# Kernel optimization log

Measured on AMD Instinct MI355X. Metric: run time of the kernel, lower is better.

The kernel has to match this reference:

```python
import jax, jax.numpy as jnp
import numpy as np
from jax import lax

Z, Y, X = 9, 5, 5          # anchor grid (AnchorInit)
A = Z * Y * X              # 225 anchors
NS = 8                     # nsample in AnchorGrouping
H = 64                     # feature / hidden width


def anchor_template():
    # (Z,Y,X,3) grid of anchor coordinates, last dim ordered (x,y,z) so that
    # anchors[:,:,:2] += g_loc shifts the planar (x,y) location.
    xs = (jnp.arange(X, dtype=jnp.float32) - (X - 1) / 2.0) * 0.2
    ys = (jnp.arange(Y, dtype=jnp.float32) - (Y - 1) / 2.0) * 0.2
    zs = jnp.arange(Z, dtype=jnp.float32) * 0.22 + 0.1
    gz, gy, gx = jnp.meshgrid(zs, ys, xs, indexing='ij')
    return jnp.stack([gx, gy, gz], axis=-1)


def setup_inputs() -> dict:
    key = jax.random.key(0)
    ks = jax.random.split(key, 16)
    B, T, N, F = 16, 64, 128, 2
    M = B * T
    s = 0.1
    f32 = jnp.float32
    return {
        'x': jax.random.normal(ks[0], (M, N, 3 + F), f32),
        'g_loc': jax.random.normal(ks[1], (B, T, 2), f32) * 0.5,
        'h0': jnp.zeros((1, B, H), f32),
        'c0': jnp.zeros((1, B, H), f32),
        # AnchorPointNet: per-point MLP 5->16->32->64 + attention pooling
        'pn_w1': jax.random.normal(ks[2], (3 + F, 16), f32) * s,
        'pn_b1': jnp.zeros((16,), f32),
        'pn_w2': jax.random.normal(ks[3], (16, 32), f32) * s,
        'pn_b2': jnp.zeros((32,), f32),
        'pn_w3': jax.random.normal(ks[4], (32, H), f32) * s,
        'pn_b3': jnp.zeros((H,), f32),
        'attn_w': jax.random.normal(ks[5], (H, 1), f32) * s,
        'attn_b': jnp.zeros((1,), f32),
        # AnchorVoxelNet: Conv3d 64->96 (3,3,3), 96->128 (3,3,3), 128->64 (5,1,1), OIDHW
        'vx_w1': jax.random.normal(ks[6], (96, 64, 3, 3, 3), f32) * s,
        'vx_b1': jnp.zeros((96,), f32),
        'vx_w2': jax.random.normal(ks[7], (128, 96, 3, 3, 3), f32) * s,
        'vx_b2': jnp.zeros((128,), f32),
        'vx_w3': jax.random.normal(ks[8], (64, 128, 5, 1, 1), f32) * s,
        'vx_b3': jnp.zeros((64,), f32),
        # AnchorRNN: 1-layer LSTM, input 64, hidden 64, torch gate order (i,f,g,o)
        'lstm_wi': jax.random.normal(ks[9], (H, 4 * H), f32) * s,
        'lstm_wh': jax.random.normal(ks[10], (H, 4 * H), f32) * s,
        'lstm_b': jnp.zeros((4 * H,), f32),
        'batch_size': 16,
        'length_size': 64,
        'feature_size': 2,
    }


def reference(x, g_loc, h0, c0,
              pn_w1, pn_b1, pn_w2, pn_b2, pn_w3, pn_b3, attn_w, attn_b,
              vx_w1, vx_b1, vx_w2, vx_b2, vx_w3, vx_b3,
              lstm_wi, lstm_wh, lstm_b,
              batch_size, length_size, feature_size):
    M = batch_size * length_size
    # ---- anchors: template grid translated by per-frame global (x,y) location
    anchors = jnp.tile(anchor_template().reshape(1, A, 3), (M, 1, 1))
    anchors = anchors.at[:, :, :2].add(g_loc.reshape(M, 1, 2))
    # ---- AnchorGrouping: 8-NN of each anchor in the radar point cloud
    xyz = x[..., :3]                      # (M,N,3)
    points = x[..., 3:]                   # (M,N,F)
    d = (jnp.sum(anchors * anchors, -1)[:, :, None]
         - 2.0 * jnp.einsum('mad,mnd->man', anchors, xyz)
         + jnp.sum(xyz * xyz, -1)[:, None, :])      # (M,A,N) squared dists
    _, idx = lax.top_k(-d, NS)                       # (M,A,8) nearest points
    bi = jnp.arange(M)[:, None, None]
    g_xyz = xyz[bi, idx] - anchors[:, :, None, :]    # (M,A,8,3) anchor-relative
    g_pts = points[bi, idx]                          # (M,A,8,F)
    grouped = jnp.concatenate([g_xyz, g_pts], -1).reshape(M * A, NS, 3 + feature_size)
    # ---- AnchorPointNet: shared MLP + attention pooling over the 8 neighbors
    f = jax.nn.relu(grouped @ pn_w1 + pn_b1)
    f = jax.nn.relu(f @ pn_w2 + pn_b2)
    f = jax.nn.relu(f @ pn_w3 + pn_b3)               # (MA,8,64)
    attn = jax.nn.softmax(f @ attn_w + attn_b, axis=1)   # (MA,8,1)
    voxel_points = jnp.sum(attn * f, axis=1)         # (MA,64)
    attn_weights = attn[..., 0]                      # (MA,8)
    # ---- AnchorVoxelNet: 3D conv over the (Z,Y,X) anchor grid
    v = voxel_points.reshape(M, Z, Y, X, H).transpose(0, 4, 1, 2, 3)  # (M,64,9,5,5)
    dn = ('NCDHW', 'OIDHW', 'NCDHW')
    v = jax.nn.relu(lax.conv_general_dilated(v, vx_w1, (1, 1, 1), 'VALID', dimension_numbers=dn)
                    + vx_b1[None, :, None, None, None])               # (M,96,7,3,3)
    v = jax.nn.relu(lax.conv_general_dilated(v, vx_w2, (1, 1, 1), 'VALID', dimension_numbers=dn)
                    + vx_b2[None, :, None, None, None])               # (M,128,5,1,1)
    v = lax.conv_general_dilated(v, vx_w3, (1, 1, 1), 'VALID', dimension_numbers=dn) \
        + vx_b3[None, :, None, None, None]                            # (M,64,1,1,1)
    voxel_vec = v.reshape(batch_size, length_size, H)
    # ---- AnchorRNN: single-layer LSTM over time
    def step(carry, xt):
        h, c = carry
        gates = xt @ lstm_wi + h @ lstm_wh + lstm_b
        i, fg, g, o = jnp.split(gates, 4, axis=-1)
        c = jax.nn.sigmoid(fg) * c + jax.nn.sigmoid(i) * jnp.tanh(g)
        h = jax.nn.sigmoid(o) * jnp.tanh(c)
        return (h, c), h
    (hn, cn), ys = lax.scan(step, (h0[0], c0[0]), voxel_vec.transpose(1, 0, 2))
    a_vec = ys.transpose(1, 0, 2)                    # (B,T,64)
    return a_vec, attn_weights, hn[None], cn[None]
```

## Files before the change

kernel.cpp:

```cpp
#include <hip/hip_runtime.h>
#include <cmath>

#define AT 225
#define NP 128
#define MT 1024
#define NSEL 8
#define HD 64

#define SZ_VOX  (1024u*64u*225u)
#define SZ_C1   (1024u*96u*63u)
#define SZ_C2   (1024u*128u*5u)
#define SZ_VV   (1024u*64u)
#define SZ_XWI  (1024u*256u)
#define SZ_W1T  (64u*27u*96u)
#define SZ_W2T  (96u*27u*128u)
#define SZ_W3T  (640u*64u)
#define SZ_W2M  (512u)

#define C2S 98

typedef __attribute__((ext_vector_type(8))) short bf16x8;
typedef __attribute__((ext_vector_type(4))) float f32x4;

__device__ __forceinline__ float sigm(float x) { return 1.0f / (1.0f + expf(-x)); }

__device__ __forceinline__ unsigned short f2bf(float f) {
    unsigned u = __float_as_uint(f);
    unsigned r = u + 0x7FFF + ((u >> 16) & 1);
    return (unsigned short)(r >> 16);
}
__device__ __forceinline__ unsigned pk2(float a, float b) {
    return (unsigned)f2bf(a) | ((unsigned)f2bf(b) << 16);
}

__global__ __launch_bounds__(256) void k_transpose(
    const float* __restrict__ w1, const float* __restrict__ w2,
    const float* __restrict__ w3, const float* __restrict__ pnw3,
    const float* __restrict__ pnw2,
    unsigned short* __restrict__ w1m, unsigned short* __restrict__ w2n,
    float* __restrict__ w3t, unsigned short* __restrict__ w3m,
    unsigned short* __restrict__ w2m)
{
    int idx = blockIdx.x * 256 + threadIdx.x;
    if (idx < 20736) {
        int lane = idx & 63, r = idx >> 6;
        int t = r % 6, s = r / 6;
        int o = t * 16 + (lane & 15);
        int kb = s * 32 + (lane >> 4) * 8;
        unsigned int dw[4];
        #pragma unroll
        for (int jd = 0; jd < 4; ++jd) {
            int k0 = kb + 2 * jd, k1 = k0 + 1;
            dw[jd] = (unsigned)f2bf(w1[o * 1728 + (k0 & 63) * 27 + (k0 >> 6)]) |
                     ((unsigned)f2bf(w1[o * 1728 + (k1 & 63) * 27 + (k1 >> 6)]) << 16);
        }
        uint4 v; v.x = dw[0]; v.y = dw[1]; v.z = dw[2]; v.w = dw[3];
        ((uint4*)w1m)[idx] = v;
    } else if (idx < 62208) {
        int q = idx - 20736;
        int lane = q & 63, r = q >> 6;
        int nt = r & 7, s = r >> 3;
        int o = nt * 16 + (lane & 15);
        int kb = s * 32 + (lane >> 4) * 8;
        unsigned int dw[4];
        #pragma unroll
        for (int jd = 0; jd < 4; ++jd) {
            int k0 = kb + 2 * jd, k1 = k0 + 1;
            dw[jd] = (unsigned)f2bf(w2[o * 2592 + (k0 % 96) * 27 + (k0 / 96)]) |
                     ((unsigned)f2bf(w2[o * 2592 + (k1 % 96) * 27 + (k1 / 96)]) << 16);
        }
        uint4 v; v.x = dw[0]; v.y = dw[1]; v.z = dw[2]; v.w = dw[3];
        ((uint4*)w2n)[q] = v;
    } else if (idx < 103168) {
        int k = idx - 62208;
        int u = k & 63, r = k >> 6;
        w3t[k] = w3[u * 640 + r];
    } else if (idx < 103424) {
        int k = idx - 103168;
        int lane = k & 63, nt = k >> 6;
        int n = nt * 16 + (lane & 15);
        int kb = (lane >> 4) * 8;
        unsigned int dw[4];
        #pragma unroll
        for (int jd = 0; jd < 4; ++jd) {
            int k0 = kb + 2 * jd;
            dw[jd] = (unsigned)f2bf(pnw3[k0 * 64 + n]) |
                     ((unsigned)f2bf(pnw3[(k0 + 1) * 64 + n]) << 16);
        }
        uint4 v; v.x = dw[0]; v.y = dw[1]; v.z = dw[2]; v.w = dw[3];
        ((uint4*)w3m)[k] = v;
    } else if (idx < 103552) {
        int k = idx - 103424;
        int lane = k & 63, nt = k >> 6;
        int n = nt * 16 + (lane & 15);
        int kb = (lane >> 4) * 8;
        unsigned int dw[4];
        #pragma unroll
        for (int jd = 0; jd < 4; ++jd) {
            int k0 = kb + 2 * jd, k1 = k0 + 1;
            float a = (k0 < 16) ? pnw2[k0 * 32 + n] : 0.0f;
            float b = (k1 < 16) ? pnw2[k1 * 32 + n] : 0.0f;
            dw[jd] = pk2(a, b);
        }
        uint4 v; v.x = dw[0]; v.y = dw[1]; v.z = dw[2]; v.w = dw[3];
        ((uint4*)w2m)[k] = v;
    }
}

__global__ __launch_bounds__(256) void k_group(
    const float* __restrict__ x, const float* __restrict__ g_loc,
    int* __restrict__ idxbuf)
{
    const int m = blockIdx.x;
    const int tid = threadIdx.x;
    __shared__ float pts[3][NP];

    for (int idx = tid; idx < NP * 5; idx += 256) {
        int n = idx / 5, c = idx % 5;
        if (c < 3) pts[c][n] = x[m * (NP * 5) + idx];
    }
    __syncthreads();

    const float gx = g_loc[m * 2 + 0], gy = g_loc[m * 2 + 1];
    const int grp = tid >> 3, li = tid & 7;

    for (int ca = 0; ca < 256; ca += 32) {
        const int a = ca + grp;
        const bool active = (a < AT);
        const int aa = active ? a : (AT - 1);
        const int azi = aa / 25, ar = aa % 25, ayi = ar / 5, axi = ar % 5;
        const float fx = ((float)axi - 2.0f) * 0.2f + gx;
        const float fy = ((float)ayi - 2.0f) * 0.2f + gy;
        const float fz = (float)azi * 0.22f + 0.1f;
        const float sa = fx * fx + fy * fy + fz * fz;

        float d[16];
        #pragma unroll
        for (int r = 0; r < 16; ++r) {
            int n = li * 16 + r;
            float px = pts[0][n], py = pts[1][n], pz = pts[2][n];
            d[r] = sa - 2.0f * (fx * px + fy * py + fz * pz)
                      + (px * px + py * py + pz * pz);
        }
        int nidx = 0;
        for (int j = 0; j < NSEL; ++j) {
            float best = 1e30f; int bidx = 0;
            #pragma unroll
            for (int r = 0; r < 16; ++r) {
                int n = li * 16 + r;
                if (d[r] < best) { best = d[r]; bidx = n; }
            }
            #pragma unroll
            for (int off = 1; off < 8; off <<= 1) {
                float ov = __shfl_xor(best, off);
                int   oi = __shfl_xor(bidx, off);
                if (ov < best || (ov == best && oi < bidx)) { best = ov; bidx = oi; }
            }
            if (li == j) nidx = bidx;
            if ((bidx >> 4) == li) {
                int slot = bidx & 15;
                #pragma unroll
                for (int r = 0; r < 16; ++r)
                    if (r == slot) d[r] = 1e30f;
            }
        }
        if (active) idxbuf[(m * AT + a) * NSEL + li] = nidx;
    }
}

__global__ __launch_bounds__(128) void k_mlpm(
    const float* __restrict__ x, const float* __restrict__ g_loc,
    const int* __restrict__ idxbuf,
    const float* __restrict__ w1, const float* __restrict__ b1,
    const unsigned short* __restrict__ w2m, const float* __restrict__ b2,
    const unsigned short* __restrict__ w3m, const float* __restrict__ b3,
    const float* __restrict__ aw, const float* __restrict__ ab,
    unsigned short* __restrict__ vox, float* __restrict__ attn_out)
{
    const int tid = threadIdx.x;
    const int row0 = blockIdx.x * 128;
    const int row = row0 + tid;

    __shared__ __align__(16) char smem[25600];
    unsigned int*   fbuf = (unsigned int*)smem;
    unsigned short* f3us = (unsigned short*)(smem + 8704);
    float*          pts  = (float*)(smem + 8704);
    float*          sbuf = (float*)smem;

    const int m0 = row0 / 1800;
    const int m1 = (row0 + 127) / 1800;
    #pragma unroll
    for (int mm = 0; mm < 2; ++mm) {
        int mload = (mm == 0) ? m0 : m1;
        for (int i = tid; i < NP * 5; i += 128) {
            int n = i / 5, c = i % 5;
            pts[(mm * 5 + c) * NP + n] = x[mload * (NP * 5) + i];
        }
    }
    __syncthreads();

    const int m = row / 1800;
    const int rr = row % 1800;
    const int a = rr >> 3;
    const int sel = (m == m0) ? 0 : 5;

    const int azi = a / 25, ar = a % 25, ayi = ar / 5, axi = ar % 5;
    const float gx = g_loc[m * 2 + 0], gy = g_loc[m * 2 + 1];
    const float fx = ((float)axi - 2.0f) * 0.2f + gx;
    const float fy = ((float)ayi - 2.0f) * 0.2f + gy;
    const float fz = (float)azi * 0.22f + 0.1f;

    const int nidx = idxbuf[row];
    const float in0 = pts[(sel + 0) * NP + nidx] - fx;
    const float in1 = pts[(sel + 1) * NP + nidx] - fy;
    const float in2 = pts[(sel + 2) * NP + nidx] - fz;
    const float in3 = pts[(sel + 3) * NP + nidx];
    const float in4 = pts[(sel + 4) * NP + nidx];

    float f1v[16];
    #pragma unroll
    for (int j = 0; j < 16; ++j) {
        float s = b1[j];
        s += in0 * w1[0 * 16 + j] + in1 * w1[1 * 16 + j] + in2 * w1[2 * 16 + j]
           + in3 * w1[3 * 16 + j] + in4 * w1[4 * 16 + j];
        f1v[j] = fmaxf(s, 0.0f);
    }
    __syncthreads();
    #pragma unroll
    for (int kd = 0; kd < 8; ++kd)
        fbuf[tid * 17 + kd] = pk2(f1v[2 * kd], f1v[2 * kd + 1]);
    #pragma unroll
    for (int kd = 8; kd < 16; ++kd)
        fbuf[tid * 17 + kd] = 0u;
    __syncthreads();

    const int wv = tid >> 6, lane = tid & 63;
    const int quad = lane >> 4, mcol = lane & 15;
    unsigned short* fus = (unsigned short*)fbuf;

    bf16x8 w2f[2];
    #pragma unroll
    for (int nt = 0; nt < 2; ++nt) {
        uint4 u = ((const uint4*)w2m)[nt * 64 + lane];
        w2f[nt] = __builtin_bit_cast(bf16x8, u);
    }
    float b2v[2] = { b2[mcol], b2[16 + mcol] };

    #pragma unroll
    for (int mt = 0; mt < 4; ++mt) {
        const int rowbase = (wv * 4 + mt) * 16;
        const int abase = (rowbase + mcol) * 17 + quad * 4;
        uint4 au;
        au.x = fbuf[abase + 0]; au.y = fbuf[abase + 1];
        au.z = fbuf[abase + 2]; au.w = fbuf[abase + 3];
        bf16x8 af = __builtin_bit_cast(bf16x8, au);
        #pragma unroll
        for (int nt = 0; nt < 2; ++nt) {
            f32x4 z = (f32x4){0.f, 0.f, 0.f, 0.f};
            f32x4 acc = __builtin_amdgcn_mfma_f32_16x16x32_bf16(af, w2f[nt], z, 0, 0, 0);
            #pragma unroll
            for (int reg = 0; reg < 4; ++reg) {
                float v = fmaxf(acc[reg] + b2v[nt], 0.0f);
                fus[(rowbase + quad * 4 + reg) * 34 + nt * 16 + mcol] = f2bf(v);
            }
        }
    }
    __syncthreads();

    bf16x8 w3f[4];
    #pragma unroll
    for (int nt = 0; nt < 4; ++nt) {
        uint4 u = ((const uint4*)w3m)[nt * 64 + lane];
        w3f[nt] = __builtin_bit_cast(bf16x8, u);
    }
    float b3v[4];
    #pragma unroll
    for (int nt = 0; nt < 4; ++nt) b3v[nt] = b3[nt * 16 + mcol];

    #pragma unroll
    for (int mt = 0; mt < 4; ++mt) {
        const int rowbase = (wv * 4 + mt) * 16;
        const int abase = (rowbase + mcol) * 17 + quad * 4;
        uint4 au;
        au.x = fbuf[abase + 0]; au.y = fbuf[abase + 1];
        au.z = fbuf[abase + 2]; au.w = fbuf[abase + 3];
        bf16x8 af = __builtin_bit_cast(bf16x8, au);
        #pragma unroll
        for (int nt = 0; nt < 4; ++nt) {
            f32x4 z = (f32x4){0.f, 0.f, 0.f, 0.f};
            f32x4 acc = __builtin_amdgcn_mfma_f32_16x16x32_bf16(af, w3f[nt], z, 0, 0, 0);
            #pragma unroll
            for (int reg = 0; reg < 4; ++reg) {
                float v = fmaxf(acc[reg] + b3v[nt], 0.0f);
                f3us[(rowbase + quad * 4 + reg) * 66 + nt * 16 + mcol] = f2bf(v);
            }
        }
    }
    __syncthreads();

    const unsigned int* f3dw = (const unsigned int*)f3us;
    float s0 = 0.f, s1 = 0.f;
    #pragma unroll
    for (int kd = 0; kd < 32; ++kd) {
        unsigned dw = f3dw[tid * 33 + kd];
        s0 = fmaf(__uint_as_float(dw << 16), aw[2 * kd], s0);
        s1 = fmaf(__uint_as_float(dw & 0xFFFF0000u), aw[2 * kd + 1], s1);
    }
    float sc = s0 + s1 + ab[0];

    float mx = sc;
    #pragma unroll
    for (int off = 1; off < 8; off <<= 1) mx = fmaxf(mx, __shfl_xor(mx, off));
    float e = expf(sc - mx);
    float den = e;
    #pragma unroll
    for (int off = 1; off < 8; off <<= 1) den += __shfl_xor(den, off);
    const float at = e / den;
    attn_out[row] = at;

    const int lgrp = tid >> 3;
    const int li = tid & 7;
    const int wl = tid & 63;
    float oo[8];
    #pragma unroll
    for (int i = 0; i < 8; ++i) oo[i] = 0.0f;
    #pragma unroll
    for (int ns = 0; ns < 8; ++ns) {
        float atn = __shfl(at, (wl >> 3) * 8 + ns);
        const int rbase = (lgrp * 8 + ns) * 33;
        #pragma unroll
        for (int q = 0; q < 4; ++q) {
            unsigned dw = f3dw[rbase + q * 8 + li];
            oo[2 * q + 0] = fmaf(atn, __uint_as_float(dw << 16), oo[2 * q + 0]);
            oo[2 * q + 1] = fmaf(atn, __uint_as_float(dw & 0xFFFF0000u), oo[2 * q + 1]);
        }
    }
    __syncthreads();
    #pragma unroll
    for (int q = 0; q < 4; ++q) {
        sbuf[lgrp * 65 + q * 16 + li * 2 + 0] = oo[2 * q + 0];
        sbuf[lgrp * 65 + q * 16 + li * 2 + 1] = oo[2 * q + 1];
    }
    __syncthreads();

    const int al = tid & 15, j = tid >> 4;
    const int ga = (row0 >> 3) + al;
    const int ma = ga / 225, aa2 = ga % 225;
    #pragma unroll
    for (int rep = 0; rep < 8; ++rep) {
        int h = j * 8 + rep;
        vox[(ma * 64 + h) * AT + aa2] = f2bf(sbuf[al * 65 + h]);
    }
}

__global__ __launch_bounds__(256) void k_conv1m(
    const unsigned short* __restrict__ vox, const unsigned short* __restrict__ w1m,
    const float* __restrict__ b1, unsigned short* __restrict__ out)
{
    const int m = blockIdx.x;
    const int tid = threadIdx.x;
    __shared__ unsigned short voxT[225 * 66];

    const unsigned int* vsrc = (const unsigned int*)(vox + (size_t)m * 14400);
    for (int i = tid; i < 7200; i += 256) {
        unsigned v = vsrc[i];
        int e0 = 2 * i, e1 = e0 + 1;
        int c0 = e0 / 225, a0 = e0 - c0 * 225;
        int c1i = e1 / 225, a1 = e1 - c1i * 225;
        voxT[a0 * 66 + c0] = (unsigned short)(v & 0xFFFFu);
        voxT[a1 * 66 + c1i] = (unsigned short)(v >> 16);
    }
    __syncthreads();

    const int wv = tid >> 6, lane = tid & 63;
    const int quad = lane >> 4, n = lane & 15;
    const int p = wv * 16 + n;
    const int pe = (p > 62) ? 62 : p;
    const int zo = pe / 9, pr = pe % 9, yo = pr / 3, xo = pr % 3;
    const int basep = zo * 25 + yo * 5 + xo;

    f32x4 acc[6];
    #pragma unroll
    for (int t = 0; t < 6; ++t) acc[t] = (f32x4){0.f, 0.f, 0.f, 0.f};

    const uint4* Aptr = (const uint4*)w1m;

    auto loadB = [&](int s) -> uint4 {
        int tap = s >> 1;
        int dz = tap / 9, tr = tap % 9, dy = tr / 3, dx = tr % 3;
        int rw = basep + dz * 25 + dy * 5 + dx;
        int bidx = rw * 66 + (s & 1) * 32 + quad * 8;
        const unsigned int* vp = (const unsigned int*)(voxT + bidx);
        uint4 r; r.x = vp[0]; r.y = vp[1]; r.z = vp[2]; r.w = vp[3];
        return r;
    };

    uint4 Acur[6], Anxt[6];
    #pragma unroll
    for (int t = 0; t < 6; ++t) Acur[t] = Aptr[t * 64 + lane];
    uint4 Bcur = loadB(0), Bnxt;

    for (int s = 0; s < 54; ++s) {
        if (s < 53) {
            Bnxt = loadB(s + 1);
            #pragma unroll
            for (int t = 0; t < 6; ++t)
                Anxt[t] = Aptr[((s + 1) * 6 + t) * 64 + lane];
        }
        bf16x8 bf = __builtin_bit_cast(bf16x8, Bcur);
        #pragma unroll
        for (int t = 0; t < 6; ++t) {
            bf16x8 af = __builtin_bit_cast(bf16x8, Acur[t]);
            acc[t] = __builtin_amdgcn_mfma_f32_16x16x32_bf16(af, bf, acc[t], 0, 0, 0);
        }
        #pragma unroll
        for (int t = 0; t < 6; ++t) Acur[t] = Anxt[t];
        Bcur = Bnxt;
    }

    if (p < 63) {
        #pragma unroll
        for (int t = 0; t < 6; ++t) {
            #pragma unroll
            for (int r = 0; r < 4; ++r) {
                int o = t * 16 + quad * 4 + r;
                out[m * (96 * 63) + o * 63 + p] =
                    f2bf(fmaxf(acc[t][r] + b1[o], 0.0f));
            }
        }
    }
}

__global__ __launch_bounds__(256) void k_conv2m(
    const unsigned short* __restrict__ c1, const unsigned short* __restrict__ w2n,
    const float* __restrict__ b2, float* __restrict__ out)
{
    const int tid = threadIdx.x;
    const int m0 = blockIdx.x * 3;
    __shared__ unsigned short c1T[3 * 63 * C2S];

    const unsigned int* csrc = (const unsigned int*)(c1 + (size_t)m0 * 6048);
    for (int i = tid; i < 9072; i += 256) {
        int e0 = 2 * i;
        int mi = e0 / 6048;
        unsigned v = (m0 + mi < MT) ? csrc[i] : 0u;
        int r0 = e0 - mi * 6048, r1 = r0 + 1;
        int o0 = r0 / 63, p0 = r0 - o0 * 63;
        int o1 = r1 / 63, p1 = r1 - o1 * 63;
        c1T[(mi * 63 + p0) * C2S + o0] = (unsigned short)(v & 0xFFFFu);
        c1T[(mi * 63 + p1) * C2S + o1] = (unsigned short)(v >> 16);
    }
    __syncthreads();

    const int wv = tid >> 6, lane = tid & 63;
    const int quad = lane >> 4, ncol = lane & 15;
    const int arow = lane & 15;
    const int mi = (arow < 15) ? arow / 5 : 2;
    const int zo = (arow < 15) ? arow % 5 : 4;

    f32x4 acc[2];
    acc[0] = (f32x4){0.f, 0.f, 0.f, 0.f};
    acc[1] = (f32x4){0.f, 0.f, 0.f, 0.f};
    const uint4* Bptr = (const uint4*)w2n;

    for (int tap = 0; tap < 27; ++tap) {
        const int dz = tap / 9, r9 = tap % 9;
        const int rowb = (mi * 63 + (zo + dz) * 9 + r9) * C2S;
        #pragma unroll
        for (int sub = 0; sub < 3; ++sub) {
            const int s = tap * 3 + sub;
            const unsigned int* ap =
                (const unsigned int*)(c1T + rowb + sub * 32 + quad * 8);
            uint4 au; au.x = ap[0]; au.y = ap[1]; au.z = ap[2]; au.w = ap[3];
            bf16x8 af = __builtin_bit_cast(bf16x8, au);
            #pragma unroll
            for (int nt = 0; nt < 2; ++nt) {
                uint4 bu = Bptr[(s * 8 + wv * 2 + nt) * 64 + lane];
                bf16x8 bf = __builtin_bit_cast(bf16x8, bu);
                acc[nt] = __builtin_amdgcn_mfma_f32_16x16x32_bf16(af, bf, acc[nt], 0, 0, 0);
            }
        }
    }

    #pragma unroll
    for (int nt = 0; nt < 2; ++nt) {
        const int o = (wv * 2 + nt) * 16 + ncol;
        const float bias = b2[o];
        #pragma unroll
        for (int reg = 0; reg < 4; ++reg) {
            int rr = quad * 4 + reg;
            if (rr < 15) {
                int mg = m0 + rr / 5;
                if (mg < MT)
                    out[mg * 640 + o * 5 + (rr % 5)] =
                        fmaxf(acc[nt][reg] + bias, 0.0f);
            }
        }
    }
}

__global__ __launch_bounds__(256) void k_c3x(
    const float* __restrict__ c2, const float* __restrict__ w3t,
    const float* __restrict__ b3, const float* __restrict__ wi,
    const float* __restrict__ lb, float* __restrict__ xwi)
{
    const int tid = threadIdx.x;
    const int m = blockIdx.x;
    __shared__ float inb[640];
    __shared__ float part[4][64];
    __shared__ float vvl[64];

    for (int i = tid; i < 640; i += 256) inb[i] = c2[m * 640 + i];
    __syncthreads();

    const int u = tid & 63, kq = tid >> 6;
    float acc = 0.0f;
    const int k0 = kq * 160;
    #pragma unroll 8
    for (int k = k0; k < k0 + 160; ++k)
        acc = fmaf(inb[k], w3t[k * 64 + u], acc);
    part[kq][u] = acc;
    __syncthreads();

    if (tid < 64)
        vvl[tid] = b3[tid] + ((part[0][tid] + part[1][tid])
                 + (part[2][tid] + part[3][tid]));
    __syncthreads();

    float a2 = lb[tid];
    #pragma unroll
    for (int k = 0; k < 64; ++k)
        a2 = fmaf(vvl[k], wi[k * 256 + tid], a2);
    xwi[m * 256 + tid] = a2;
}

__global__ __launch_bounds__(256) void k_lstm(
    const float* __restrict__ xwi, const float* __restrict__ whg,
    const float* __restrict__ h0, const float* __restrict__ c0,
    float* __restrict__ avec, float* __restrict__ hn, float* __restrict__ cn)
{
    const int b = blockIdx.x;
    const int j = threadIdx.x;
    __shared__ float hbuf[64];
    __shared__ float gbuf[256];

    float wh[64];
    #pragma unroll
    for (int k = 0; k < 64; ++k) wh[k] = whg[k * 256 + j];

    if (j < 64) hbuf[j] = h0[b * 64 + j];
    float c = (j < 64) ? c0[b * 64 + j] : 0.0f;
    __syncthreads();

    for (int t = 0; t < 64; ++t) {
        float g = xwi[(b * 64 + t) * 256 + j];
        #pragma unroll
        for (int k = 0; k < 64; ++k) g = fmaf(hbuf[k], wh[k], g);
        gbuf[j] = g;
        __syncthreads();
        if (j < 64) {
            float gi = gbuf[j], gf = gbuf[64 + j], gg = gbuf[128 + j], go = gbuf[192 + j];
            c = sigm(gf) * c + sigm(gi) * tanhf(gg);
            float h = sigm(go) * tanhf(c);
            hbuf[j] = h;
            avec[(b * 64 + t) * 64 + j] = h;
        }
        __syncthreads();
    }
    if (j < 64) {
        hn[b * 64 + j] = hbuf[j];
        cn[b * 64 + j] = c;
    }
}

extern "C" void kernel_launch(void* const* d_in, const int* in_sizes, int n_in,
                              void* d_out, int out_size, void* d_ws, size_t ws_size,
                              hipStream_t stream) {
    const float* x     = (const float*)d_in[0];
    const float* g_loc = (const float*)d_in[1];
    const float* h0    = (const float*)d_in[2];
    const float* c0    = (const float*)d_in[3];
    const float* pn_w1 = (const float*)d_in[4];
    const float* pn_b1 = (const float*)d_in[5];
    const float* pn_w2 = (const float*)d_in[6];
    const float* pn_b2 = (const float*)d_in[7];
    const float* pn_w3 = (const float*)d_in[8];
    const float* pn_b3 = (const float*)d_in[9];
    const float* aw    = (const float*)d_in[10];
    const float* ab    = (const float*)d_in[11];
    const float* vx_w1 = (const float*)d_in[12];
    const float* vx_b1 = (const float*)d_in[13];
    const float* vx_w2 = (const float*)d_in[14];
    const float* vx_b2 = (const float*)d_in[15];
    const float* vx_w3 = (const float*)d_in[16];
    const float* vx_b3 = (const float*)d_in[17];
    const float* lwi   = (const float*)d_in[18];
    const float* lwh   = (const float*)d_in[19];
    const float* lb    = (const float*)d_in[20];

    float* ws  = (float*)d_ws;
    float* voxr = ws;
    float* c1r  = voxr + SZ_VOX;
    float* c2  = c1r + SZ_C1;
    float* vv  = c2 + SZ_C2;
    float* xwi = vv + SZ_VV;
    float* w1r = xwi + SZ_XWI;
    float* w2r = w1r + SZ_W1T;
    float* w3t = w2r + SZ_W2T;
    float* w2mr = w3t + SZ_W3T;
    unsigned short* voxh = (unsigned short*)voxr;
    unsigned short* c1h  = (unsigned short*)c1r;
    unsigned short* w1m = (unsigned short*)w1r;
    unsigned short* w2n = (unsigned short*)w2r;
    unsigned short* w2m = (unsigned short*)w2mr;
    unsigned short* w3m = (unsigned short*)xwi;
    int*   idxb = (int*)c1r;

    float* out   = (float*)d_out;
    float* avec  = out;
    float* attnw = out + 65536;
    float* hn    = out + 65536 + 1843200;
    float* cn    = hn + 1024;

    k_transpose<<<405, 256, 0, stream>>>(vx_w1, vx_w2, vx_w3, pn_w3, pn_w2,
                                         w1m, w2n, w3t, w3m, w2m);
    k_group<<<1024, 256, 0, stream>>>(x, g_loc, idxb);
    k_mlpm<<<14400, 128, 0, stream>>>(x, g_loc, idxb, pn_w1, pn_b1, w2m, pn_b2,
                                      w3m, pn_b3, aw, ab, voxh, attnw);
    k_conv1m<<<1024, 256, 0, stream>>>(voxh, w1m, vx_b1, c1h);
    k_conv2m<<<342, 256, 0, stream>>>(c1h, w2n, vx_b2, c2);
    k_c3x<<<1024, 256, 0, stream>>>(c2, w3t, vx_b3, lwi, lb, xwi);
    k_lstm<<<16, 256, 0, stream>>>(xwi, lwh, h0, c0, avec, hn, cn);
}
```

Measured before the change: 387.8 us.

## Tune several kernels: hardware bf16 pack, deeper conv1 prefetch, smaller conv2 tiles, vectorized LSTM

```diff
diff --git a/kernel.cpp b/kernel.cpp
--- a/kernel.cpp
+++ b/kernel.cpp
@@ -29,8 +29,20 @@
     unsigned r = u + 0x7FFF + ((u >> 16) & 1);
     return (unsigned short)(r >> 16);
 }
+
+#if defined(__has_builtin)
+#if __has_builtin(__builtin_amdgcn_cvt_pk_bf16_f32)
+#define HAVE_CVT_PK_BF16 1
+#endif
+#endif
+
 __device__ __forceinline__ unsigned pk2(float a, float b) {
+#ifdef HAVE_CVT_PK_BF16
+    auto v = __builtin_amdgcn_cvt_pk_bf16_f32(a, b);
+    return __builtin_bit_cast(unsigned, v);
+#else
     return (unsigned)f2bf(a) | ((unsigned)f2bf(b) << 16);
+#endif
 }
 
 __global__ __launch_bounds__(256) void k_transpose(
@@ -100,7 +112,7 @@
             int k0 = kb + 2 * jd, k1 = k0 + 1;
             float a = (k0 < 16) ? pnw2[k0 * 32 + n] : 0.0f;
             float b = (k1 < 16) ? pnw2[k1 * 32 + n] : 0.0f;
-            dw[jd] = pk2(a, b);
+            dw[jd] = (unsigned)f2bf(a) | ((unsigned)f2bf(b) << 16);
         }
         uint4 v; v.x = dw[0]; v.y = dw[1]; v.z = dw[2]; v.w = dw[3];
         ((uint4*)w2m)[k] = v;
@@ -190,19 +202,16 @@
     const int m0 = row0 / 1800;
     const int m1 = (row0 + 127) / 1800;
     #pragma unroll
-    for (int mm = 0; mm < 2; ++mm) {
-        int mload = (mm == 0) ? m0 : m1;
-        for (int i = tid; i < NP * 5; i += 128) {
-            int n = i / 5, c = i % 5;
-            pts[(mm * 5 + c) * NP + n] = x[mload * (NP * 5) + i];
-        }
+    for (int i = tid; i < 640; i += 128) {
+        pts[i]       = x[m0 * 640 + i];
+        pts[640 + i] = x[m1 * 640 + i];
     }
     __syncthreads();
 
     const int m = row / 1800;
     const int rr = row % 1800;
     const int a = rr >> 3;
-    const int sel = (m == m0) ? 0 : 5;
+    const int base = (m == m0) ? 0 : 640;
 
     const int azi = a / 25, ar = a % 25, ayi = ar / 5, axi = ar % 5;
     const float gx = g_loc[m * 2 + 0], gy = g_loc[m * 2 + 1];
@@ -211,11 +220,11 @@
     const float fz = (float)azi * 0.22f + 0.1f;
 
     const int nidx = idxbuf[row];
-    const float in0 = pts[(sel + 0) * NP + nidx] - fx;
-    const float in1 = pts[(sel + 1) * NP + nidx] - fy;
-    const float in2 = pts[(sel + 2) * NP + nidx] - fz;
-    const float in3 = pts[(sel + 3) * NP + nidx];
-    const float in4 = pts[(sel + 4) * NP + nidx];
+    const float in0 = pts[base + nidx * 5 + 0] - fx;
+    const float in1 = pts[base + nidx * 5 + 1] - fy;
+    const float in2 = pts[base + nidx * 5 + 2] - fz;
+    const float in3 = pts[base + nidx * 5 + 3];
+    const float in4 = pts[base + nidx * 5 + 4];
 
     float f1v[16];
     #pragma unroll
@@ -395,27 +404,31 @@
         return r;
     };
 
-    uint4 Acur[6], Anxt[6];
-    #pragma unroll
-    for (int t = 0; t < 6; ++t) Acur[t] = Aptr[t * 64 + lane];
-    uint4 Bcur = loadB(0), Bnxt;
+    uint4 A0[6], A1[6], A2[6];
+    uint4 B0, B1, B2;
+    #pragma unroll
+    for (int t = 0; t < 6; ++t) {
+        A0[t] = Aptr[(0 * 6 + t) * 64 + lane];
+        A1[t] = Aptr[(1 * 6 + t) * 64 + lane];
+    }
+    B0 = loadB(0); B1 = loadB(1);
 
     for (int s = 0; s < 54; ++s) {
-        if (s < 53) {
-            Bnxt = loadB(s + 1);
+        if (s < 52) {
+            B2 = loadB(s + 2);
             #pragma unroll
             for (int t = 0; t < 6; ++t)
-                Anxt[t] = Aptr[((s + 1) * 6 + t) * 64 + lane];
-        }
-        bf16x8 bf = __builtin_bit_cast(bf16x8, Bcur);
+                A2[t] = Aptr[((s + 2) * 6 + t) * 64 + lane];
+        }
+        bf16x8 bf = __builtin_bit_cast(bf16x8, B0);
         #pragma unroll
         for (int t = 0; t < 6; ++t) {
-            bf16x8 af = __builtin_bit_cast(bf16x8, Acur[t]);
+            bf16x8 af = __builtin_bit_cast(bf16x8, A0[t]);
             acc[t] = __builtin_amdgcn_mfma_f32_16x16x32_bf16(af, bf, acc[t], 0, 0, 0);
         }
         #pragma unroll
-        for (int t = 0; t < 6; ++t) Acur[t] = Anxt[t];
-        Bcur = Bnxt;
+        for (int t = 0; t < 6; ++t) { A0[t] = A1[t]; A1[t] = A2[t]; }
+        B0 = B1; B1 = B2;
     }
 
     if (p < 63) {
@@ -436,14 +449,14 @@
     const float* __restrict__ b2, float* __restrict__ out)
 {
     const int tid = threadIdx.x;
-    const int m0 = blockIdx.x * 3;
-    __shared__ unsigned short c1T[3 * 63 * C2S];
+    const int m0 = blockIdx.x * 2;
+    __shared__ unsigned short c1T[2 * 63 * C2S];
 
     const unsigned int* csrc = (const unsigned int*)(c1 + (size_t)m0 * 6048);
-    for (int i = tid; i < 9072; i += 256) {
+    for (int i = tid; i < 6048; i += 256) {
+        unsigned v = csrc[i];
         int e0 = 2 * i;
-        int mi = e0 / 6048;
-        unsigned v = (m0 + mi < MT) ? csrc[i] : 0u;
+        int mi = (i >= 3024);
         int r0 = e0 - mi * 6048, r1 = r0 + 1;
         int o0 = r0 / 63, p0 = r0 - o0 * 63;
         int o1 = r1 / 63, p1 = r1 - o1 * 63;
@@ -455,8 +468,8 @@
     const int wv = tid >> 6, lane = tid & 63;
     const int quad = lane >> 4, ncol = lane & 15;
     const int arow = lane & 15;
-    const int mi = (arow < 15) ? arow / 5 : 2;
-    const int zo = (arow < 15) ? arow % 5 : 4;
+    const int mi = (arow < 10) ? arow / 5 : 1;
+    const int zo = (arow < 10) ? arow % 5 : 4;
 
     f32x4 acc[2];
     acc[0] = (f32x4){0.f, 0.f, 0.f, 0.f};
@@ -489,11 +502,10 @@
         #pragma unroll
         for (int reg = 0; reg < 4; ++reg) {
             int rr = quad * 4 + reg;
-            if (rr < 15) {
+            if (rr < 10) {
                 int mg = m0 + rr / 5;
-                if (mg < MT)
-                    out[mg * 640 + o * 5 + (rr % 5)] =
-                        fmaxf(acc[nt][reg] + bias, 0.0f);
+                out[mg * 640 + o * 5 + (rr % 5)] =
+                    fmaxf(acc[nt][reg] + bias, 0.0f);
             }
         }
     }
@@ -541,7 +553,7 @@
 {
     const int b = blockIdx.x;
     const int j = threadIdx.x;
-    __shared__ float hbuf[64];
+    __shared__ __align__(16) float hbuf[64];
     __shared__ float gbuf[256];
 
     float wh[64];
@@ -552,10 +564,17 @@
     float c = (j < 64) ? c0[b * 64 + j] : 0.0f;
     __syncthreads();
 
+    const float4* hb4 = (const float4*)hbuf;
     for (int t = 0; t < 64; ++t) {
         float g = xwi[(b * 64 + t) * 256 + j];
         #pragma unroll
-        for (int k = 0; k < 64; ++k) g = fmaf(hbuf[k], wh[k], g);
+        for (int k4 = 0; k4 < 16; ++k4) {
+            float4 h4 = hb4[k4];
+            g = fmaf(h4.x, wh[4 * k4 + 0], g);
+            g = fmaf(h4.y, wh[4 * k4 + 1], g);
+            g = fmaf(h4.z, wh[4 * k4 + 2], g);
+            g = fmaf(h4.w, wh[4 * k4 + 3], g);
+        }
         gbuf[j] = g;
         __syncthreads();
         if (j < 64) {
@@ -628,7 +647,7 @@
     k_mlpm<<<14400, 128, 0, stream>>>(x, g_loc, idxb, pn_w1, pn_b1, w2m, pn_b2,
                                       w3m, pn_b3, aw, ab, voxh, attnw);
     k_conv1m<<<1024, 256, 0, stream>>>(voxh, w1m, vx_b1, c1h);
-    k_conv2m<<<342, 256, 0, stream>>>(c1h, w2n, vx_b2, c2);
+    k_conv2m<<<512, 256, 0, stream>>>(c1h, w2n, vx_b2, c2);
     k_c3x<<<1024, 256, 0, stream>>>(c2, w3t, vx_b3, lwi, lb, xwi);
     k_lstm<<<16, 256, 0, stream>>>(xwi, lwh, h0, c0, avec, hn, cn);
 }
```

Measured after the change: 378.4 us. 1.02x faster.
